# Performance work log

Measured on AMD Instinct MI355X. Metric: run time of the kernel, lower is better.

The kernel has to match this reference:

```python
import jax, jax.numpy as jnp
import numpy as np

BN_EPS = 1e-6


def _conv1x1(x, w, b):
    # x: (B, Cin, N, K), w: (Cout, Cin), b: (Cout,)
    return jnp.einsum('oc,bcnk->bonk', w, x) + b[None, :, None, None]


def _bn(x, gamma, beta, mean, var):
    # inference-mode BatchNorm2d over channel axis 1
    inv = gamma / jnp.sqrt(var + BN_EPS)
    return x * inv[None, :, None, None] + (beta - mean * inv)[None, :, None, None]


def setup_inputs() -> dict:
    key = jax.random.key(0)
    ks = jax.random.split(key, 12)
    B, N, K = 4, 16384, 16
    C_out = 32
    C_img = 2 * C_out - 10          # 54, so concat has 2*C_out = 64 channels
    C_in1 = 2 * C_out               # 64
    C_in2 = 2 * (C_out + 3)         # 70

    points = jax.random.normal(ks[0], (B, N, 3), jnp.float32)
    image_features = jax.random.normal(ks[1], (B, C_img, N, K), jnp.float32)
    dist = jax.random.uniform(ks[2], (B, N, K), jnp.float32)
    idx = jax.random.randint(ks[3], (B, N, K), 0, N, dtype=jnp.int32)

    w1 = jax.random.normal(ks[4], (C_out, C_in1), jnp.float32) / np.sqrt(C_in1).astype(np.float32)
    b1 = jnp.zeros((C_out,), jnp.float32)
    gamma1 = jnp.ones((C_out,), jnp.float32)
    beta1 = jnp.zeros((C_out,), jnp.float32)
    mean1 = 0.1 * jax.random.normal(ks[5], (C_out,), jnp.float32)
    var1 = 0.5 + jax.random.uniform(ks[6], (C_out,), jnp.float32)

    w2 = jax.random.normal(ks[7], (C_out, C_in2), jnp.float32) / np.sqrt(C_in2).astype(np.float32)
    b2 = jnp.zeros((C_out,), jnp.float32)
    gamma2 = jnp.ones((C_out,), jnp.float32)
    beta2 = jnp.zeros((C_out,), jnp.float32)
    mean2 = 0.1 * jax.random.normal(ks[8], (C_out,), jnp.float32)
    var2 = 0.5 + jax.random.uniform(ks[9], (C_out,), jnp.float32)

    return {
        'points': points, 'image_features': image_features, 'dist': dist, 'idx': idx,
        'w1': w1, 'b1': b1, 'gamma1': gamma1, 'beta1': beta1, 'mean1': mean1, 'var1': var1,
        'w2': w2, 'b2': b2, 'gamma2': gamma2, 'beta2': beta2, 'mean2': mean2, 'var2': var2,
    }


def reference(points, image_features, dist, idx,
              w1, b1, gamma1, beta1, mean1, var1,
              w2, b2, gamma2, beta2, mean2, var2):
    B, N, K = idx.shape
    pts = jnp.swapaxes(points, 1, 2)                       # (B, 3, N)
    ep = jnp.broadcast_to(pts[:, :, :, None], (B, 3, N, K))  # extended points
    # KNN gather: nb[b, c, n, k] = pts[b, c, idx[b, n, k]]
    nb = jax.vmap(lambda p, i: p[:, i])(pts, idx)          # (B, 3, N, K)

    concat = jnp.concatenate(
        [ep, nb, ep - nb, dist[:, None, :, :], image_features], axis=1)  # (B, 64, N, K)

    h = jax.nn.relu(_bn(_conv1x1(concat, w1, b1), gamma1, beta1, mean1, var1))  # (B, 32, N, K)
    feat = jnp.concatenate([h, ep], axis=1)                # (B, 35, N, K)

    pooled = jnp.concatenate(
        [jnp.max(feat, axis=-1, keepdims=True),
         jnp.mean(feat, axis=-1, keepdims=True)], axis=1)  # (B, 70, N, 1)

    out = jax.nn.relu(_bn(_conv1x1(pooled, w2, b2), gamma2, beta2, mean2, var2))  # (B, 32, N, 1)
    return out
```

## Files before the change

kernel.cpp:

```cpp
#include <hip/hip_runtime.h>
#include <hip/hip_bf16.h>
#include <cmath>

#define BN_EPS 1e-6f
typedef unsigned int u32;
typedef __attribute__((ext_vector_type(8))) short short8;
typedef __attribute__((ext_vector_type(4))) float f32x4;

constexpr int B_    = 4;
constexpr int N_    = 16384;
constexpr int K_    = 16;
constexpr int C_IMG = 54;
constexpr int C1    = 64;
constexpr int CO    = 32;
constexpr int C2    = 70;
constexpr int NK    = N_ * K_;

constexpr int NTB   = 64;
constexpr int NSTEP = 8;
constexpr int SN    = 8;
constexpr int SPOS  = 128;
constexpr int BPOS  = 1024;
constexpr int IST   = 260;
constexpr int CST   = 1028;
constexpr int TPB   = N_ / NTB;
constexpr int NBLK  = B_ * TPB;

__device__ inline u32 pkbf(float a, float b) {
    union { __hip_bfloat162 h; u32 u; } cv;
    cv.h = __float22bfloat162_rn(make_float2(a, b));
    return cv.u;
}

__device__ inline void dma16(const float* gsrc, float* ldst) {
    __builtin_amdgcn_global_load_lds(
        (const __attribute__((address_space(1))) void*)gsrc,
        (__attribute__((address_space(3))) void*)ldst, 16, 0, 0);
}

__global__ __launch_bounds__(256, 2) void pif_mfma_kernel(
    const float* __restrict__ points, const float* __restrict__ imgf,
    const float* __restrict__ dist,   const int*   __restrict__ idx,
    const float* __restrict__ w1, const float* __restrict__ b1,
    const float* __restrict__ g1, const float* __restrict__ be1,
    const float* __restrict__ m1, const float* __restrict__ v1,
    const float* __restrict__ w2, const float* __restrict__ b2,
    const float* __restrict__ g2, const float* __restrict__ be2,
    const float* __restrict__ m2, const float* __restrict__ v2,
    float* __restrict__ out)
{
    __shared__ float imgf_lds[2][27][IST];
    __shared__ u32   comp_lds[5][CST];
    __shared__ float pooled[SN][77];

    const int t = threadIdx.x;

    const int g   = blockIdx.x;
    const int sw  = (g & 7) * (NBLK / 8) + (g >> 3);
    const int b   = sw / TPB;
    const int bn0 = (sw % TPB) * NTB;

    const int lane = t & 63, w = t >> 6;
    const int m16 = lane & 15, quad = lane >> 4;

    const int cp0 = (w < 3) ? w * 7 : 21;
    const int ncp = (w < 3) ? 7 : 6;
    const float* ib = imgf + (size_t)b * C_IMG * NK;
    const int laneHi = lane >> 5, lane31 = lane & 31;

    {
        const int off0 = bn0 * K_;
        for (int i = 0; i < ncp; ++i) {
            const int cp = cp0 + i;
            const float* gs = ib + (size_t)(2 * cp + laneHi) * NK + off0 + lane31 * 4;
            dma16(gs, &imgf_lds[0][cp][0]);
        }
    }

    #pragma unroll
    for (int c2 = 0; c2 < 4; ++c2) {
        const int pos = c2 * 256 + t;
        const int nl = pos >> 4, kk = pos & 15;
        const int gn = bn0 + nl;
        const int ii = (b * N_ + gn) * K_ + kk;
        const int jx = idx[ii];
        const float dvv = dist[ii];
        const int pbo = (b * N_ + gn) * 3;
        const float px = points[pbo], py = points[pbo + 1], pz = points[pbo + 2];
        const int qbo = (b * N_ + jx) * 3;
        const float qx = points[qbo], qy = points[qbo + 1], qz = points[qbo + 2];
        comp_lds[0][pos] = pkbf(px, py);
        comp_lds[1][pos] = pkbf(pz, qx);
        comp_lds[2][pos] = pkbf(qy, qz);
        comp_lds[3][pos] = pkbf(px - qx, py - qy);
        comp_lds[4][pos] = pkbf(pz - qz, dvv);
    }

    short8 bfrag[2][2];
    float  inv1v[2], add1v[2];
    #pragma unroll
    for (int ot = 0; ot < 2; ++ot) {
        const int o = ot * 16 + m16;
        #pragma unroll
        for (int kc = 0; kc < 2; ++kc) {
            union { u32 u[4]; short8 v; } bf;
            #pragma unroll
            for (int i2 = 0; i2 < 4; ++i2) {
                const int lc0 = kc * 32 + quad * 8 + 2 * i2, lc1 = lc0 + 1;
                const int c0 = (lc0 < 54) ? (10 + lc0) : (lc0 - 54);
                const int c1 = (lc1 < 54) ? (10 + lc1) : (lc1 - 54);
                bf.u[i2] = pkbf(w1[o * C1 + c0], w1[o * C1 + c1]);
            }
            bfrag[ot][kc] = bf.v;
        }
        const float iv = g1[o] * rsqrtf(v1[o] + BN_EPS);
        inv1v[ot] = iv;
        add1v[ot] = be1[o] - m1[o] * iv + b1[o] * iv;
    }

    const int nnC = t & 7, oC = t >> 3;
    const float iv2 = g2[oC] * rsqrtf(v2[oC] + BN_EPS);
    const float ad2 = be2[oC] - m2[oC] * iv2;
    const float bb2 = b2[oC];
    const float* wr2 = w2 + oC * C2;

    __syncthreads();

    #pragma unroll 1
    for (int s = 0; s < NSTEP; ++s) {
        const int bb = s & 1;

        if (s + 1 < NSTEP) {
            const int offn = (bn0 + (s + 1) * SN) * K_;
            for (int i = 0; i < ncp; ++i) {
                const int cp = cp0 + i;
                const float* gs = ib + (size_t)(2 * cp + laneHi) * NK + offn + lane31 * 4;
                dma16(gs, &imgf_lds[bb ^ 1][cp][0]);
            }
            if (w < 3) asm volatile("s_waitcnt vmcnt(7)" ::: "memory");
            else       asm volatile("s_waitcnt vmcnt(6)" ::: "memory");
        } else {
            asm volatile("s_waitcnt vmcnt(0)" ::: "memory");
        }
        __builtin_amdgcn_s_barrier();
        __builtin_amdgcn_sched_barrier(0);

        if (t < 24) {
            const int jj = t >> 3, nn2 = t & 7;
            const float v = points[(b * N_ + bn0 + s * SN + nn2) * 3 + jj];
            pooled[nn2][32 + jj] = v;
            pooled[nn2][67 + jj] = v;
        }

        const float* Xi = &imgf_lds[bb][0][0];
        const int pco = s * SPOS;

        #pragma unroll
        for (int u = 0; u < 2; ++u) {
            const int m = 2 * w + u;
            const int p = m * 16 + m16;
            f32x4 acc0 = (f32x4){0.f, 0.f, 0.f, 0.f};
            f32x4 acc1 = (f32x4){0.f, 0.f, 0.f, 0.f};

            #pragma unroll
            for (int kc = 0; kc < 2; ++kc) {
                union { u32 uu[4]; short8 v; } af;
                if (kc == 0) {
                    #pragma unroll
                    for (int i2 = 0; i2 < 4; ++i2) {
                        const float* cb = Xi + (quad * 4 + i2) * IST + p;
                        af.uu[i2] = pkbf(cb[0], cb[128]);
                    }
                } else {
                    if (quad < 2) {
                        #pragma unroll
                        for (int i2 = 0; i2 < 4; ++i2) {
                            const float* cb = Xi + (16 + quad * 4 + i2) * IST + p;
                            af.uu[i2] = pkbf(cb[0], cb[128]);
                        }
                    } else if (quad == 2) {
                        #pragma unroll
                        for (int i2 = 0; i2 < 3; ++i2) {
                            const float* cb = Xi + (24 + i2) * IST + p;
                            af.uu[i2] = pkbf(cb[0], cb[128]);
                        }
                        af.uu[3] = comp_lds[0][pco + p];
                    } else {
                        #pragma unroll
                        for (int i2 = 0; i2 < 4; ++i2)
                            af.uu[i2] = comp_lds[1 + i2][pco + p];
                    }
                }
                acc0 = __builtin_amdgcn_mfma_f32_16x16x32_bf16(af.v, bfrag[0][kc], acc0, 0, 0, 0);
                acc1 = __builtin_amdgcn_mfma_f32_16x16x32_bf16(af.v, bfrag[1][kc], acc1, 0, 0, 0);
            }

            #pragma unroll
            for (int ot = 0; ot < 2; ++ot) {
                const f32x4 aa = ot ? acc1 : acc0;
                float mx = 0.f, sm = 0.f;
                #pragma unroll
                for (int r = 0; r < 4; ++r) {
                    float hv = fmaf(aa[r], inv1v[ot], add1v[ot]);
                    hv = fmaxf(hv, 0.f);
                    mx = fmaxf(mx, hv);
                    sm += hv;
                }
                mx = fmaxf(mx, __shfl_xor(mx, 16));
                mx = fmaxf(mx, __shfl_xor(mx, 32));
                sm += __shfl_xor(sm, 16);
                sm += __shfl_xor(sm, 32);
                if (quad == 0) {
                    pooled[m][ot * 16 + m16]      = mx;
                    pooled[m][35 + ot * 16 + m16] = sm * (1.f / 16.f);
                }
            }
        }

        asm volatile("s_waitcnt lgkmcnt(0)" ::: "memory");
        __builtin_amdgcn_s_barrier();
        __builtin_amdgcn_sched_barrier(0);

        {
            float a0 = 0.f, a1 = 0.f;
            #pragma unroll
            for (int c = 0; c < C2; c += 2) {
                a0 = fmaf(wr2[c],     pooled[nnC][c],     a0);
                a1 = fmaf(wr2[c + 1], pooled[nnC][c + 1], a1);
            }
            float ov = fmaf((a0 + a1) + bb2, iv2, ad2);
            ov = fmaxf(ov, 0.f);
            out[(b * CO + oC) * N_ + bn0 + s * SN + nnC] = ov;
        }

        asm volatile("s_waitcnt lgkmcnt(0)" ::: "memory");
        __builtin_amdgcn_s_barrier();
        __builtin_amdgcn_sched_barrier(0);
    }
}

extern "C" void kernel_launch(void* const* d_in, const int* in_sizes, int n_in,
                              void* d_out, int out_size, void* d_ws, size_t ws_size,
                              hipStream_t stream) {
    const float* points = (const float*)d_in[0];
    const float* imgf   = (const float*)d_in[1];
    const float* dist   = (const float*)d_in[2];
    const int*   idx    = (const int*)  d_in[3];
    const float* w1     = (const float*)d_in[4];
    const float* b1     = (const float*)d_in[5];
    const float* g1     = (const float*)d_in[6];
    const float* be1    = (const float*)d_in[7];
    const float* m1     = (const float*)d_in[8];
    const float* v1     = (const float*)d_in[9];
    const float* w2     = (const float*)d_in[10];
    const float* b2     = (const float*)d_in[11];
    const float* g2     = (const float*)d_in[12];
    const float* be2    = (const float*)d_in[13];
    const float* m2     = (const float*)d_in[14];
    const float* v2     = (const float*)d_in[15];
    float* out          = (float*)d_out;

    pif_mfma_kernel<<<NBLK, 256, 0, stream>>>(
        points, imgf, dist, idx,
        w1, b1, g1, be1, m1, v1,
        w2, b2, g2, be2, m2, v2, out);
}
```

Before: 362.2 us.

## Stage image features through registers as packed bf16 and defer second conv to epilogue

Replaces the direct global-to-LDS DMA of fp32 image features with register-staged loads two steps ahead, packing channel pairs to bf16 before writing to LDS. This halves LDS footprint and removes per-element conversion in the MFMA operand load. The second 1x1 conv now runs once after all steps over a 64-point pooled buffer, which drops one barrier per step. The trade-off is more registers held for prefetch and a scalar-broadcast w2 epilogue loop.

```diff
diff --git a/kernel.cpp b/kernel.cpp
--- a/kernel.cpp
+++ b/kernel.cpp
@@ -18,11 +18,11 @@
 
 constexpr int NTB   = 64;
 constexpr int NSTEP = 8;
-constexpr int SN    = 8;
 constexpr int SPOS  = 128;
-constexpr int BPOS  = 1024;
-constexpr int IST   = 260;
+constexpr int XR    = 132;
+constexpr int XBUFB = 27 * XR * 4;
 constexpr int CST   = 1028;
+constexpr int PST   = 73;
 constexpr int TPB   = N_ / NTB;
 constexpr int NBLK  = B_ * TPB;
 
@@ -30,12 +30,6 @@
     union { __hip_bfloat162 h; u32 u; } cv;
     cv.h = __float22bfloat162_rn(make_float2(a, b));
     return cv.u;
-}
-
-__device__ inline void dma16(const float* gsrc, float* ldst) {
-    __builtin_amdgcn_global_load_lds(
-        (const __attribute__((address_space(1))) void*)gsrc,
-        (__attribute__((address_space(3))) void*)ldst, 16, 0, 0);
 }
 
 __global__ __launch_bounds__(256, 2) void pif_mfma_kernel(
@@ -49,13 +43,12 @@
     const float* __restrict__ m2, const float* __restrict__ v2,
     float* __restrict__ out)
 {
-    __shared__ float imgf_lds[2][27][IST];
+    __shared__ __align__(16) u32 xbuf[2][27][XR];
     __shared__ u32   comp_lds[5][CST];
-    __shared__ float pooled[SN][77];
+    __shared__ float pooled_all[NTB][PST];
 
     const int t = threadIdx.x;
-
-    const int g   = blockIdx.x;
+    const int g = blockIdx.x;
     const int sw  = (g & 7) * (NBLK / 8) + (g >> 3);
     const int b   = sw / TPB;
     const int bn0 = (sw % TPB) * NTB;
@@ -63,19 +56,30 @@
     const int lane = t & 63, w = t >> 6;
     const int m16 = lane & 15, quad = lane >> 4;
 
-    const int cp0 = (w < 3) ? w * 7 : 21;
-    const int ncp = (w < 3) ? 7 : 6;
-    const float* ib = imgf + (size_t)b * C_IMG * NK;
-    const int laneHi = lane >> 5, lane31 = lane & 31;
-
-    {
-        const int off0 = bn0 * K_;
-        for (int i = 0; i < ncp; ++i) {
-            const int cp = cp0 + i;
-            const float* gs = ib + (size_t)(2 * cp + laneHi) * NK + off0 + lane31 * 4;
-            dma16(gs, &imgf_lds[0][cp][0]);
-        }
-    }
+    const float* ib = imgf + (size_t)b * C_IMG * NK + bn0 * K_;
+    const float* gp0[4]; const float* gp1[4]; u32* lw[4];
+    #pragma unroll
+    for (int jj = 0; jj < 4; ++jj) {
+        const int item = w * 216 + ((jj < 3) ? jj * 64 + lane : 192 + lane);
+        const int cp = item >> 5, q = item & 31;
+        gp0[jj] = ib + (size_t)(2 * cp) * NK + 4 * q;
+        gp1[jj] = ib + (size_t)(2 * cp + 1) * NK + 4 * q;
+        lw[jj]  = &xbuf[0][cp][4 * q];
+    }
+
+    float4 rA[4][2], rB[4][2];
+    #pragma unroll
+    for (int jj = 0; jj < 4; ++jj)
+        if (jj < 3 || lane < 24) {
+            rA[jj][0] = *(const float4*)(gp0[jj]);
+            rA[jj][1] = *(const float4*)(gp1[jj]);
+        }
+    #pragma unroll
+    for (int jj = 0; jj < 4; ++jj)
+        if (jj < 3 || lane < 24) {
+            rB[jj][0] = *(const float4*)(gp0[jj] + SPOS);
+            rB[jj][1] = *(const float4*)(gp1[jj] + SPOS);
+        }
 
     #pragma unroll
     for (int c2 = 0; c2 < 4; ++c2) {
@@ -95,6 +99,12 @@
         comp_lds[3][pos] = pkbf(px - qx, py - qy);
         comp_lds[4][pos] = pkbf(pz - qz, dvv);
     }
+    if (t < 192) {
+        const int nn = t & 63, jj = t >> 6;
+        const float v = points[(b * N_ + bn0 + nn) * 3 + jj];
+        pooled_all[nn][32 + jj] = v;
+        pooled_all[nn][67 + jj] = v;
+    }
 
     short8 bfrag[2][2];
     float  inv1v[2], add1v[2];
@@ -118,124 +128,138 @@
         add1v[ot] = be1[o] - m1[o] * iv + b1[o] * iv;
     }
 
-    const int nnC = t & 7, oC = t >> 3;
-    const float iv2 = g2[oC] * rsqrtf(v2[oC] + BN_EPS);
-    const float ad2 = be2[oC] - m2[oC] * iv2;
-    const float bb2 = b2[oC];
-    const float* wr2 = w2 + oC * C2;
+    #pragma unroll
+    for (int jj = 0; jj < 4; ++jj)
+        if (jj < 3 || lane < 24) {
+            uint4 pk;
+            pk.x = pkbf(rA[jj][0].x, rA[jj][1].x);
+            pk.y = pkbf(rA[jj][0].y, rA[jj][1].y);
+            pk.z = pkbf(rA[jj][0].z, rA[jj][1].z);
+            pk.w = pkbf(rA[jj][0].w, rA[jj][1].w);
+            *(uint4*)lw[jj] = pk;
+        }
 
     __syncthreads();
 
-    #pragma unroll 1
-    for (int s = 0; s < NSTEP; ++s) {
-        const int bb = s & 1;
-
-        if (s + 1 < NSTEP) {
-            const int offn = (bn0 + (s + 1) * SN) * K_;
-            for (int i = 0; i < ncp; ++i) {
-                const int cp = cp0 + i;
-                const float* gs = ib + (size_t)(2 * cp + laneHi) * NK + offn + lane31 * 4;
-                dma16(gs, &imgf_lds[bb ^ 1][cp][0]);
-            }
-            if (w < 3) asm volatile("s_waitcnt vmcnt(7)" ::: "memory");
-            else       asm volatile("s_waitcnt vmcnt(6)" ::: "memory");
-        } else {
-            asm volatile("s_waitcnt vmcnt(0)" ::: "memory");
-        }
-        __builtin_amdgcn_s_barrier();
-        __builtin_amdgcn_sched_barrier(0);
-
-        if (t < 24) {
-            const int jj = t >> 3, nn2 = t & 7;
-            const float v = points[(b * N_ + bn0 + s * SN + nn2) * 3 + jj];
-            pooled[nn2][32 + jj] = v;
-            pooled[nn2][67 + jj] = v;
-        }
-
-        const float* Xi = &imgf_lds[bb][0][0];
-        const int pco = s * SPOS;
-
+#define PIF_COMPUTE(S)                                                         \
+    {                                                                          \
+        const u32* Xi = &xbuf[(S) & 1][0][0];                                  \
+        _Pragma("unroll")                                                      \
+        for (int u = 0; u < 2; ++u) {                                          \
+            const int m = 2 * w + u;                                           \
+            const int p = m * 16 + m16;                                        \
+            f32x4 acc0 = (f32x4){0.f, 0.f, 0.f, 0.f};                          \
+            f32x4 acc1 = (f32x4){0.f, 0.f, 0.f, 0.f};                          \
+            {                                                                  \
+                union { u32 uu[4]; short8 v; } af;                             \
+                _Pragma("unroll")                                              \
+                for (int i2 = 0; i2 < 4; ++i2)                                 \
+                    af.uu[i2] = Xi[(quad * 4 + i2) * XR + p];                   \
+                acc0 = __builtin_amdgcn_mfma_f32_16x16x32_bf16(af.v, bfrag[0][0], acc0, 0, 0, 0); \
+                acc1 = __builtin_amdgcn_mfma_f32_16x16x32_bf16(af.v, bfrag[1][0], acc1, 0, 0, 0); \
+            }                                                                  \
+            {                                                                  \
+                union { u32 uu[4]; short8 v; } af;                             \
+                if (quad < 2) {                                                \
+                    _Pragma("unroll")                                          \
+                    for (int i2 = 0; i2 < 4; ++i2)                             \
+                        af.uu[i2] = Xi[(16 + quad * 4 + i2) * XR + p];          \
+                } else if (quad == 2) {                                        \
+                    _Pragma("unroll")                                          \
+                    for (int i2 = 0; i2 < 3; ++i2)                             \
+                        af.uu[i2] = Xi[(24 + i2) * XR + p];                     \
+                    af.uu[3] = comp_lds[0][(S) * SPOS + p];                    \
+                } else {                                                       \
+                    _Pragma("unroll")                                          \
+                    for (int i2 = 0; i2 < 4; ++i2)                             \
+                        af.uu[i2] = comp_lds[1 + i2][(S) * SPOS + p];          \
+                }                                                              \
+                acc0 = __builtin_amdgcn_mfma_f32_16x16x32_bf16(af.v, bfrag[0][1], acc0, 0, 0, 0); \
+                acc1 = __builtin_amdgcn_mfma_f32_16x16x32_bf16(af.v, bfrag[1][1], acc1, 0, 0, 0); \
+            }                                                                  \
+            _Pragma("unroll")                                                  \
+            for (int ot = 0; ot < 2; ++ot) {                                   \
+                const f32x4 aa = ot ? acc1 : acc0;                             \
+                float mx = 0.f, sm = 0.f;                                      \
+                _Pragma("unroll")                                              \
+                for (int r = 0; r < 4; ++r) {                                  \
+                    float hv = fmaf(aa[r], inv1v[ot], add1v[ot]);              \
+                    hv = fmaxf(hv, 0.f);                                       \
+                    mx = fmaxf(mx, hv);                                        \
+                    sm += hv;                                                  \
+                }                                                              \
+                mx = fmaxf(mx, __shfl_xor(mx, 16));                            \
+                mx = fmaxf(mx, __shfl_xor(mx, 32));                            \
+                sm += __shfl_xor(sm, 16);                                      \
+                sm += __shfl_xor(sm, 32);                                      \
+                if (quad == 0) {                                               \
+                    pooled_all[(S) * 8 + m][ot * 16 + m16]      = mx;          \
+                    pooled_all[(S) * 8 + m][35 + ot * 16 + m16] = sm * (1.f / 16.f); \
+                }                                                              \
+            }                                                                  \
+        }                                                                      \
+    }
+
+#define PIF_STEP(S, RISS, RPK)                                                 \
+    {                                                                          \
+        if ((S) + 2 < NSTEP) {                                                 \
+            _Pragma("unroll")                                                  \
+            for (int jj = 0; jj < 4; ++jj)                                     \
+                if (jj < 3 || lane < 24) {                                     \
+                    RISS[jj][0] = *(const float4*)(gp0[jj] + ((S) + 2) * SPOS);\
+                    RISS[jj][1] = *(const float4*)(gp1[jj] + ((S) + 2) * SPOS);\
+                }                                                              \
+            asm volatile("s_waitcnt vmcnt(8)" ::: "memory");                   \
+        } else if ((S) + 1 < NSTEP) {                                          \
+            asm volatile("s_waitcnt vmcnt(0)" ::: "memory");                   \
+        }                                                                      \
+        if ((S) + 1 < NSTEP) {                                                 \
+            _Pragma("unroll")                                                  \
+            for (int jj = 0; jj < 4; ++jj)                                     \
+                if (jj < 3 || lane < 24) {                                     \
+                    uint4 pk;                                                  \
+                    pk.x = pkbf(RPK[jj][0].x, RPK[jj][1].x);                   \
+                    pk.y = pkbf(RPK[jj][0].y, RPK[jj][1].y);                   \
+                    pk.z = pkbf(RPK[jj][0].z, RPK[jj][1].z);                   \
+                    pk.w = pkbf(RPK[jj][0].w, RPK[jj][1].w);                   \
+                    *(uint4*)((char*)lw[jj] + (((S) + 1) & 1) * XBUFB) = pk;   \
+                }                                                              \
+        }                                                                      \
+        PIF_COMPUTE(S);                                                        \
+        asm volatile("s_waitcnt lgkmcnt(0)" ::: "memory");                     \
+        __builtin_amdgcn_s_barrier();                                          \
+        __builtin_amdgcn_sched_barrier(0);                                     \
+    }
+
+    PIF_STEP(0, rA, rB)
+    PIF_STEP(1, rB, rA)
+    PIF_STEP(2, rA, rB)
+    PIF_STEP(3, rB, rA)
+    PIF_STEP(4, rA, rB)
+    PIF_STEP(5, rB, rA)
+    PIF_STEP(6, rA, rB)
+    PIF_STEP(7, rB, rA)
+
+#undef PIF_STEP
+#undef PIF_COMPUTE
+
+    const int wu = __builtin_amdgcn_readfirstlane(w);
+    float accE[8];
+    #pragma unroll
+    for (int oo = 0; oo < 8; ++oo) accE[oo] = 0.f;
+    for (int c = 0; c < C2; ++c) {
+        const float rv = pooled_all[lane][c];
         #pragma unroll
-        for (int u = 0; u < 2; ++u) {
-            const int m = 2 * w + u;
-            const int p = m * 16 + m16;
-            f32x4 acc0 = (f32x4){0.f, 0.f, 0.f, 0.f};
-            f32x4 acc1 = (f32x4){0.f, 0.f, 0.f, 0.f};
-
-            #pragma unroll
-            for (int kc = 0; kc < 2; ++kc) {
-                union { u32 uu[4]; short8 v; } af;
-                if (kc == 0) {
-                    #pragma unroll
-                    for (int i2 = 0; i2 < 4; ++i2) {
-                        const float* cb = Xi + (quad * 4 + i2) * IST + p;
-                        af.uu[i2] = pkbf(cb[0], cb[128]);
-                    }
-                } else {
-                    if (quad < 2) {
-                        #pragma unroll
-                        for (int i2 = 0; i2 < 4; ++i2) {
-                            const float* cb = Xi + (16 + quad * 4 + i2) * IST + p;
-                            af.uu[i2] = pkbf(cb[0], cb[128]);
-                        }
-                    } else if (quad == 2) {
-                        #pragma unroll
-                        for (int i2 = 0; i2 < 3; ++i2) {
-                            const float* cb = Xi + (24 + i2) * IST + p;
-                            af.uu[i2] = pkbf(cb[0], cb[128]);
-                        }
-                        af.uu[3] = comp_lds[0][pco + p];
-                    } else {
-                        #pragma unroll
-                        for (int i2 = 0; i2 < 4; ++i2)
-                            af.uu[i2] = comp_lds[1 + i2][pco + p];
-                    }
-                }
-                acc0 = __builtin_amdgcn_mfma_f32_16x16x32_bf16(af.v, bfrag[0][kc], acc0, 0, 0, 0);
-                acc1 = __builtin_amdgcn_mfma_f32_16x16x32_bf16(af.v, bfrag[1][kc], acc1, 0, 0, 0);
-            }
-
-            #pragma unroll
-            for (int ot = 0; ot < 2; ++ot) {
-                const f32x4 aa = ot ? acc1 : acc0;
-                float mx = 0.f, sm = 0.f;
-                #pragma unroll
-                for (int r = 0; r < 4; ++r) {
-                    float hv = fmaf(aa[r], inv1v[ot], add1v[ot]);
-                    hv = fmaxf(hv, 0.f);
-                    mx = fmaxf(mx, hv);
-                    sm += hv;
-                }
-                mx = fmaxf(mx, __shfl_xor(mx, 16));
-                mx = fmaxf(mx, __shfl_xor(mx, 32));
-                sm += __shfl_xor(sm, 16);
-                sm += __shfl_xor(sm, 32);
-                if (quad == 0) {
-                    pooled[m][ot * 16 + m16]      = mx;
-                    pooled[m][35 + ot * 16 + m16] = sm * (1.f / 16.f);
-                }
-            }
-        }
-
-        asm volatile("s_waitcnt lgkmcnt(0)" ::: "memory");
-        __builtin_amdgcn_s_barrier();
-        __builtin_amdgcn_sched_barrier(0);
-
-        {
-            float a0 = 0.f, a1 = 0.f;
-            #pragma unroll
-            for (int c = 0; c < C2; c += 2) {
-                a0 = fmaf(wr2[c],     pooled[nnC][c],     a0);
-                a1 = fmaf(wr2[c + 1], pooled[nnC][c + 1], a1);
-            }
-            float ov = fmaf((a0 + a1) + bb2, iv2, ad2);
-            ov = fmaxf(ov, 0.f);
-            out[(b * CO + oC) * N_ + bn0 + s * SN + nnC] = ov;
-        }
-
-        asm volatile("s_waitcnt lgkmcnt(0)" ::: "memory");
-        __builtin_amdgcn_s_barrier();
-        __builtin_amdgcn_sched_barrier(0);
+        for (int oo = 0; oo < 8; ++oo)
+            accE[oo] = fmaf(w2[(8 * wu + oo) * C2 + c], rv, accE[oo]);
+    }
+    #pragma unroll
+    for (int oo = 0; oo < 8; ++oo) {
+        const int o = 8 * wu + oo;
+        const float iv2 = g2[o] * rsqrtf(v2[o] + BN_EPS);
+        float ov = fmaf(accE[oo] + b2[o], iv2, be2[o] - m2[o] * iv2);
+        ov = fmaxf(ov, 0.f);
+        out[(b * CO + o) * N_ + bn0 + lane] = ov;
     }
 }
 
```

New measurement: 363.7 us. About the same (+0.4%).
